# Kernel optimization log

Hardware: AMD Instinct MI355X
Metric: run time of the kernel (lower is better)

Reference implementation:

```python
import jax, jax.numpy as jnp
import numpy as np

N = 8192
LATENT_DIM = 64


def setup_inputs() -> dict:
    key = jax.random.key(0)
    kx, ky = jax.random.split(key)
    x = jax.random.normal(kx, (N, LATENT_DIM), dtype=jnp.float32)
    y = jax.random.normal(ky, (N, LATENT_DIM), dtype=jnp.float32)
    return {"x": x, "y": y}


def _rbf_kernel(a, b):
    # Faithful to torch: exp(-mean((a_i - b_j)^2, axis=dim) / dim)
    #                  = exp(-||a_i - b_j||^2 / dim^2)
    # Computed via the expanded-sq-dist identity to avoid the [N, N, dim]
    # tiled intermediate the torch code materializes.
    dim = a.shape[1]
    sq_a = jnp.sum(a * a, axis=1)  # [Na]
    sq_b = jnp.sum(b * b, axis=1)  # [Nb]
    sq_dist = sq_a[:, None] + sq_b[None, :] - 2.0 * (a @ b.T)  # [Na, Nb]
    return jnp.exp(-sq_dist / (dim * dim))


def reference(x, y):
    # MMD with RBF kernel: mean k(x,x) + mean k(y,y) - 2 mean k(x,y)
    kxx = jnp.mean(_rbf_kernel(x, x))
    kyy = jnp.mean(_rbf_kernel(y, y))
    kxy = jnp.mean(_rbf_kernel(x, y))
    return kxx + kyy - 2.0 * kxy
```

## Files before the change

kernel.cpp:

```cpp
#include <hip/hip_runtime.h>
#include <cmath>

#define NPTS 8192
#define DIM 64
#define BT 128

#define LEAF_F   0
#define LEAF_N   (3 * 8192 * 64)
#define ROWS_F   (LEAF_F + LEAF_N)
#define ROWS_N   (3 * 8192)
#define MEANS_F  (ROWS_F + ROWS_N)
#define NX_F     ((MEANS_F + 3 + 3) & ~3)
#define NY_F     (NX_F + 8192)
#define SPLIT_F  (NY_F + 8192)
#define SPLIT_ELEMS (NPTS * DIM)


typedef short bf16x8 __attribute__((ext_vector_type(8)));
typedef float f32x4  __attribute__((ext_vector_type(4)));

__device__ __forceinline__ unsigned short f32_bf16_rne(float f) {
    unsigned u = __float_as_uint(f);
    return (unsigned short)((u + 0x7FFFu + ((u >> 16) & 1u)) >> 16);
}
__device__ __forceinline__ float bf16_f32(unsigned short h) {
    return __uint_as_float(((unsigned)h) << 16);
}

__device__ __forceinline__ float exp2_hw(float x) {
#if __has_builtin(__builtin_amdgcn_exp2f)
    return __builtin_amdgcn_exp2f(x);
#else
    float r;
    asm("v_exp_f32 %0, %1" : "=v"(r) : "v"(x));
    return r;
#endif
}

#define SWZ_XOR1(x)  __int_as_float(__builtin_amdgcn_ds_swizzle(__float_as_int(x), 0x041F))
#define SWZ_XOR2(x)  __int_as_float(__builtin_amdgcn_ds_swizzle(__float_as_int(x), 0x081F))
#define SWZ_XOR4(x)  __int_as_float(__builtin_amdgcn_ds_swizzle(__float_as_int(x), 0x101F))
#define SWZ_XOR8(x)  __int_as_float(__builtin_amdgcn_ds_swizzle(__float_as_int(x), 0x201F))
#define SWZ_XOR16(x) __int_as_float(__builtin_amdgcn_ds_swizzle(__float_as_int(x), 0x401F))

__global__ void prep_kernel(const float* __restrict__ x, const float* __restrict__ y,
                            unsigned short* __restrict__ Xh, unsigned short* __restrict__ Xl,
                            unsigned short* __restrict__ Yh, unsigned short* __restrict__ Yl,
                            float* __restrict__ nx, float* __restrict__ ny) {
    int gtid = blockIdx.x * 256 + threadIdx.x;
    int r  = gtid >> 4;
    int k4 = gtid & 15;
    int isY = r >= NPTS;
    int rr = isY ? r - NPTS : r;
    const float4* Rg = (const float4*)((isY ? y : x) + (size_t)rr * DIM);
    unsigned short* Hh = isY ? Yh : Xh;
    unsigned short* Hl = isY ? Yl : Xl;
    const int t16 = rr >> 4, mrow = rr & 15;
    float4 v = Rg[k4];
    ushort4 h, l;
    h.x = f32_bf16_rne(v.x); l.x = f32_bf16_rne(v.x - bf16_f32(h.x));
    h.y = f32_bf16_rne(v.y); l.y = f32_bf16_rne(v.y - bf16_f32(h.y));
    h.z = f32_bf16_rne(v.z); l.z = f32_bf16_rne(v.z - bf16_f32(h.z));
    h.w = f32_bf16_rne(v.w); l.w = f32_bf16_rne(v.w - bf16_f32(h.w));
    int off = t16 * 1024 + (k4 >> 3) * 512 + ((k4 >> 1) & 3) * 128 + mrow * 8 + (k4 & 1) * 4;
    *(ushort4*)(Hh + off) = h;
    *(ushort4*)(Hl + off) = l;
    float s = v.x * v.x;
    s = fmaf(v.y, v.y, s); s = fmaf(v.z, v.z, s); s = fmaf(v.w, v.w, s);
    s = s + SWZ_XOR1(s);
    s = s + SWZ_XOR2(s);
    s = s + SWZ_XOR4(s);
    s = s + SWZ_XOR8(s);
    if (k4 == 0) { if (isY) ny[rr] = s; else nx[rr] = s; }
}

__global__ __launch_bounds__(512, 3) void mmd_tile_kernel(
    const unsigned short* __restrict__ Xh, const unsigned short* __restrict__ Xl,
    const unsigned short* __restrict__ Yh, const unsigned short* __restrict__ Yl,
    const float* __restrict__ nx, const float* __restrict__ ny,
    float* __restrict__ leafs)
{
    int id  = blockIdx.x + 65 * (blockIdx.y + 64 * blockIdx.z);
    int nid = (id & 7) * 1040 + (id >> 3);
    int zb  = nid >= 4160;
    int rem = nid - zb * 4160;
    int gj  = rem / 65;
    int gi  = rem - gj * 65;

    int zz, bx, by;
    if (zb == 1) {
        if (gi >= 64) return;
        zz = 2; bx = gi; by = gj;
    } else if (gi > gj) {
        zz = 0; by = gj; bx = gi - 1;
    } else {
        zz = 1; by = gi; bx = gj;
    }

    __shared__ float rowpart[2][BT];
    __shared__ float colpart[4][BT];

    const int t = threadIdx.x;
    const size_t arow = (size_t)by * BT;
    const size_t brow = (size_t)bx * BT;
    const int cb = bx;

    const unsigned short* pAh = (zz == 1) ? Yh : Xh;
    const unsigned short* pAl = (zz == 1) ? Yl : Xl;
    const unsigned short* pBh = (zz == 0) ? Xh : Yh;
    const unsigned short* pBl = (zz == 0) ? Xl : Yl;
    const float* nA = (zz == 1) ? ny : nx;
    const float* nB = (zz == 0) ? nx : ny;

    const int lane = t & 63;
    const int wv   = t >> 6;
    const int mrow = lane & 15;
    const int quad = lane >> 4;
    const int rblk = (wv & 3) << 5;
    const int cblk = (wv >> 2) << 6;

    const int aT = by * 8 + (wv & 3) * 2;
    const int bT = bx * 8 + (wv >> 2) * 4;
    const int lsub = quad * 128 + mrow * 8;

    const bool domirror = (zz < 2) && (bx > by);

    float sa[8];
    #pragma unroll
    for (int rt = 0; rt < 2; ++rt)
        #pragma unroll
        for (int i = 0; i < 4; ++i)
            sa[rt * 4 + i] = nA[arow + rblk + rt * 16 + quad * 4 + i];
    float sb[4];
    #pragma unroll
    for (int ct = 0; ct < 4; ++ct)
        sb[ct] = nB[brow + cblk + ct * 16 + mrow];

    bf16x8 fAh[2][2], fAl[2][2];
    #pragma unroll
    for (int rt = 0; rt < 2; ++rt)
        #pragma unroll
        for (int kc = 0; kc < 2; ++kc) {
            int off = (aT + rt) * 1024 + kc * 512 + lsub;
            fAh[rt][kc] = *(const bf16x8*)(pAh + off);
            fAl[rt][kc] = *(const bf16x8*)(pAl + off);
        }

    bf16x8 fBh0[4], fBh1[4], fBl0[4], fBl1[4];
    #pragma unroll
    for (int ct = 0; ct < 4; ++ct) {
        int boff = (bT + ct) * 1024 + lsub;
        fBh0[ct] = *(const bf16x8*)(pBh + boff);
        fBh1[ct] = *(const bf16x8*)(pBh + boff + 512);
        fBl0[ct] = *(const bf16x8*)(pBl + boff);
        fBl1[ct] = *(const bf16x8*)(pBl + boff + 512);
    }

    const float SCL = (float)(-1.4426950408889634 / 4096.0);
    float rs01[2][4] = {{0.f,0.f,0.f,0.f},{0.f,0.f,0.f,0.f}};
    float rs23[2][4] = {{0.f,0.f,0.f,0.f},{0.f,0.f,0.f,0.f}};
    float cs[4];

    #pragma unroll
    for (int ct = 0; ct < 4; ++ct) {
        bf16x8 bh0 = fBh0[ct];
        bf16x8 bh1 = fBh1[ct];
        bf16x8 bl0 = fBl0[ct];
        bf16x8 bl1 = fBl1[ct];

        f32x4 c0 = (f32x4){0.f, 0.f, 0.f, 0.f};
        f32x4 c1 = (f32x4){0.f, 0.f, 0.f, 0.f};
        __builtin_amdgcn_s_setprio(1);
        c0 = __builtin_amdgcn_mfma_f32_16x16x32_bf16(fAh[0][0], bh0, c0, 0, 0, 0);
        c0 = __builtin_amdgcn_mfma_f32_16x16x32_bf16(fAh[0][0], bl0, c0, 0, 0, 0);
        c0 = __builtin_amdgcn_mfma_f32_16x16x32_bf16(fAl[0][0], bh0, c0, 0, 0, 0);
        c0 = __builtin_amdgcn_mfma_f32_16x16x32_bf16(fAh[0][1], bh1, c0, 0, 0, 0);
        c0 = __builtin_amdgcn_mfma_f32_16x16x32_bf16(fAh[0][1], bl1, c0, 0, 0, 0);
        c0 = __builtin_amdgcn_mfma_f32_16x16x32_bf16(fAl[0][1], bh1, c0, 0, 0, 0);
        c1 = __builtin_amdgcn_mfma_f32_16x16x32_bf16(fAh[1][0], bh0, c1, 0, 0, 0);
        c1 = __builtin_amdgcn_mfma_f32_16x16x32_bf16(fAh[1][0], bl0, c1, 0, 0, 0);
        c1 = __builtin_amdgcn_mfma_f32_16x16x32_bf16(fAl[1][0], bh0, c1, 0, 0, 0);
        c1 = __builtin_amdgcn_mfma_f32_16x16x32_bf16(fAh[1][1], bh1, c1, 0, 0, 0);
        c1 = __builtin_amdgcn_mfma_f32_16x16x32_bf16(fAh[1][1], bl1, c1, 0, 0, 0);
        c1 = __builtin_amdgcn_mfma_f32_16x16x32_bf16(fAl[1][1], bh1, c1, 0, 0, 0);
        __builtin_amdgcn_s_setprio(0);

        float k0[4], k1[4];
        #pragma unroll
        for (int i = 0; i < 4; ++i) {
            float d0  = c0[i];
            float s20 = sa[i] + sb[ct];
            k0[i] = exp2_hw((s20 - 2.0f * d0) * SCL);
            float d1  = c1[i];
            float s21 = sa[4 + i] + sb[ct];
            k1[i] = exp2_hw((s21 - 2.0f * d1) * SCL);
        }
        if (ct < 2) {
            #pragma unroll
            for (int i = 0; i < 4; ++i) { rs01[0][i] += k0[i]; rs01[1][i] += k1[i]; }
        } else {
            #pragma unroll
            for (int i = 0; i < 4; ++i) { rs23[0][i] += k0[i]; rs23[1][i] += k1[i]; }
        }
        if (domirror)
            cs[ct] = ((k0[0] + k0[1]) + (k0[2] + k0[3]))
                   + ((k1[0] + k1[1]) + (k1[2] + k1[3]));
    }

    float rs[2][4];
    #pragma unroll
    for (int rt = 0; rt < 2; ++rt)
        #pragma unroll
        for (int i = 0; i < 4; ++i)
            rs[rt][i] = rs01[rt][i] + rs23[rt][i];

    const int b0 = lane & 1;
    const int b1 = (lane >> 1) & 1;
    const int b2 = (lane >> 2) & 1;
    const int b3 = (lane >> 3) & 1;

    float a4[4];
    #pragma unroll
    for (int i = 0; i < 4; ++i) {
        float snd = b3 ? rs[0][i] : rs[1][i];
        float rcv = SWZ_XOR8(snd);
        a4[i] = (b3 ? rs[1][i] : rs[0][i]) + rcv;
    }
    float a2[2];
    #pragma unroll
    for (int j = 0; j < 2; ++j) {
        float snd = b2 ? a4[j] : a4[2 + j];
        float rcv = SWZ_XOR4(snd);
        a2[j] = (b2 ? a4[2 + j] : a4[j]) + rcv;
    }
    {
        float snd = b1 ? a2[0] : a2[1];
        float rcv = SWZ_XOR2(snd);
        float a1  = (b1 ? a2[1] : a2[0]) + rcv;
        float r64 = a1 + SWZ_XOR1(a1);
        if (b0 == 0)
            rowpart[wv >> 2][rblk + b3 * 16 + quad * 4 + b2 * 2 + b1] = r64;
    }

    if (domirror) {
        const int b4 = (lane >> 4) & 1;
        const int b5 = (lane >> 5) & 1;
        float c2[2];
        #pragma unroll
        for (int j = 0; j < 2; ++j) {
            float snd = b4 ? cs[j] : cs[2 + j];
            float rcv = SWZ_XOR16(snd);
            c2[j] = (b4 ? cs[2 + j] : cs[j]) + rcv;
        }
        float snd = b5 ? c2[0] : c2[1];
        float rcv = __shfl_xor(snd, 32);
        float c1v = (b5 ? c2[1] : c2[0]) + rcv;
        colpart[wv & 3][cblk + (b4 * 2 + b5) * 16 + mrow] = c1v;
    }
    __syncthreads();

    if (t < BT) {
        leafs[((size_t)zz * 64 + cb) * 8192 + arow + t] = rowpart[0][t] + rowpart[1][t];
        if (domirror) {
            leafs[((size_t)zz * 64 + by) * 8192 + brow + t] =
                (colpart[0][t] + colpart[1][t]) + (colpart[2][t] + colpart[3][t]);
        }
    }
}

__global__ void rowsum_kernel(const float* __restrict__ leafs, float* __restrict__ rowsums) {
    const int t = threadIdx.x;
    const int wv = t >> 6;
    const int lane = t & 63;
    const int p = lane >> 4;
    const int rlo = lane & 15;
    const int gr = blockIdx.x * 64 + wv * 16 + rlo;
    const int z = gr >> 13;
    const int r = gr & 8191;
    const float* base = leafs + ((size_t)z * 64 + p * 16) * 8192 + r;
    float v[16];
    #pragma unroll
    for (int i = 0; i < 16; ++i) v[i] = base[(size_t)i * 8192];
    #pragma unroll
    for (int n = 8; n >= 1; n >>= 1)
        #pragma unroll
        for (int i = 0; i < 16; ++i)
            if (i < n) v[i] = v[2*i] + v[2*i+1];
    float s = v[0];
    float u = s + SWZ_XOR16(s);
    float w = u + __shfl_xor(u, 32);
    if (p == 0) rowsums[gr] = w;
}

__global__ void colsum_kernel(const float* __restrict__ rowsums, float* __restrict__ out) {
    __shared__ float L[256];
    __shared__ float m[3];
    const int t = threadIdx.x;
    for (int z = 0; z < 3; ++z) {
        const float4* src = (const float4*)(rowsums + z * 8192);
        float w[32];
        #pragma unroll
        for (int i = 0; i < 8; ++i) {
            float4 q = src[t * 8 + i];
            w[4*i+0] = q.x; w[4*i+1] = q.y; w[4*i+2] = q.z; w[4*i+3] = q.w;
        }
        #pragma unroll
        for (int n = 16; n >= 1; n >>= 1)
            #pragma unroll
            for (int i = 0; i < 32; ++i)
                if (i < n) w[i] = w[2*i] + w[2*i+1];
        L[t] = w[0];
        __syncthreads();
        for (int n = 128; n >= 1; n >>= 1) {
            float u = 0.f;
            if (t < n) u = L[2*t] + L[2*t+1];
            __syncthreads();
            if (t < n) L[t] = u;
            __syncthreads();
        }
        if (t == 0) m[z] = L[0] * (1.0f / 67108864.0f);
        __syncthreads();
    }
    if (t == 0) {
        float t1 = m[0] + m[1];
        out[0] = t1 - 2.0f * m[2];
    }
}

extern "C" void kernel_launch(void* const* d_in, const int* in_sizes, int n_in,
                              void* d_out, int out_size, void* d_ws, size_t ws_size,
                              hipStream_t stream) {
    const float* x = (const float*)d_in[0];
    const float* y = (const float*)d_in[1];
    float* wsf     = (float*)d_ws;
    float* leafs   = wsf + LEAF_F;
    float* rowsums = wsf + ROWS_F;
    float* nx      = wsf + NX_F;
    float* ny      = wsf + NY_F;
    unsigned short* Xh = (unsigned short*)(wsf + SPLIT_F);
    unsigned short* Xl = Xh + SPLIT_ELEMS;
    unsigned short* Yh = Xl + SPLIT_ELEMS;
    unsigned short* Yl = Yh + SPLIT_ELEMS;

    prep_kernel<<<1024, 256, 0, stream>>>(x, y, Xh, Xl, Yh, Yl, nx, ny);
    dim3 grid(65, 64, 2);
    mmd_tile_kernel<<<grid, 512, 0, stream>>>(Xh, Xl, Yh, Yl, nx, ny, leafs);
    rowsum_kernel<<<384, 256, 0, stream>>>(leafs, rowsums);
    colsum_kernel<<<1, 256, 0, stream>>>(rowsums, (float*)d_out);
}
```

Before: 130.5 us.

## Double-buffer B fragments, raise occupancy bound, parallelize colsum over three sums

The tile kernel no longer preloads all four column-tiles of B fragments into registers. It keeps only the current fragment set and prefetches the next one each iteration, and the launch bound is raised from 3 to 6 blocks per SM, both to cut register pressure and allow more waves in flight. The final colsum kernel now reduces the three row-sum arrays concurrently with 768 threads instead of looping over them serially. The tighter register budget risks spills or less latency hiding per wave.

```diff
diff --git a/kernel.cpp b/kernel.cpp
--- a/kernel.cpp
+++ b/kernel.cpp
@@ -74,7 +74,7 @@
     if (k4 == 0) { if (isY) ny[rr] = s; else nx[rr] = s; }
 }
 
-__global__ __launch_bounds__(512, 3) void mmd_tile_kernel(
+__global__ __launch_bounds__(512, 6) void mmd_tile_kernel(
     const unsigned short* __restrict__ Xh, const unsigned short* __restrict__ Xl,
     const unsigned short* __restrict__ Yh, const unsigned short* __restrict__ Yl,
     const float* __restrict__ nx, const float* __restrict__ ny,
@@ -146,43 +146,43 @@
             fAl[rt][kc] = *(const bf16x8*)(pAl + off);
         }
 
-    bf16x8 fBh0[4], fBh1[4], fBl0[4], fBl1[4];
-    #pragma unroll
-    for (int ct = 0; ct < 4; ++ct) {
-        int boff = (bT + ct) * 1024 + lsub;
-        fBh0[ct] = *(const bf16x8*)(pBh + boff);
-        fBh1[ct] = *(const bf16x8*)(pBh + boff + 512);
-        fBl0[ct] = *(const bf16x8*)(pBl + boff);
-        fBl1[ct] = *(const bf16x8*)(pBl + boff + 512);
-    }
-
     const float SCL = (float)(-1.4426950408889634 / 4096.0);
     float rs01[2][4] = {{0.f,0.f,0.f,0.f},{0.f,0.f,0.f,0.f}};
     float rs23[2][4] = {{0.f,0.f,0.f,0.f},{0.f,0.f,0.f,0.f}};
     float cs[4];
 
+    const int boff0 = bT * 1024 + lsub;
+    bf16x8 cbh0 = *(const bf16x8*)(pBh + boff0);
+    bf16x8 cbh1 = *(const bf16x8*)(pBh + boff0 + 512);
+    bf16x8 cbl0 = *(const bf16x8*)(pBl + boff0);
+    bf16x8 cbl1 = *(const bf16x8*)(pBl + boff0 + 512);
+
     #pragma unroll
     for (int ct = 0; ct < 4; ++ct) {
-        bf16x8 bh0 = fBh0[ct];
-        bf16x8 bh1 = fBh1[ct];
-        bf16x8 bl0 = fBl0[ct];
-        bf16x8 bl1 = fBl1[ct];
+        bf16x8 nbh0, nbh1, nbl0, nbl1;
+        if (ct < 3) {
+            int boff = (bT + ct + 1) * 1024 + lsub;
+            nbh0 = *(const bf16x8*)(pBh + boff);
+            nbh1 = *(const bf16x8*)(pBh + boff + 512);
+            nbl0 = *(const bf16x8*)(pBl + boff);
+            nbl1 = *(const bf16x8*)(pBl + boff + 512);
+        }
 
         f32x4 c0 = (f32x4){0.f, 0.f, 0.f, 0.f};
         f32x4 c1 = (f32x4){0.f, 0.f, 0.f, 0.f};
         __builtin_amdgcn_s_setprio(1);
-        c0 = __builtin_amdgcn_mfma_f32_16x16x32_bf16(fAh[0][0], bh0, c0, 0, 0, 0);
-        c0 = __builtin_amdgcn_mfma_f32_16x16x32_bf16(fAh[0][0], bl0, c0, 0, 0, 0);
-        c0 = __builtin_amdgcn_mfma_f32_16x16x32_bf16(fAl[0][0], bh0, c0, 0, 0, 0);
-        c0 = __builtin_amdgcn_mfma_f32_16x16x32_bf16(fAh[0][1], bh1, c0, 0, 0, 0);
-        c0 = __builtin_amdgcn_mfma_f32_16x16x32_bf16(fAh[0][1], bl1, c0, 0, 0, 0);
-        c0 = __builtin_amdgcn_mfma_f32_16x16x32_bf16(fAl[0][1], bh1, c0, 0, 0, 0);
-        c1 = __builtin_amdgcn_mfma_f32_16x16x32_bf16(fAh[1][0], bh0, c1, 0, 0, 0);
-        c1 = __builtin_amdgcn_mfma_f32_16x16x32_bf16(fAh[1][0], bl0, c1, 0, 0, 0);
-        c1 = __builtin_amdgcn_mfma_f32_16x16x32_bf16(fAl[1][0], bh0, c1, 0, 0, 0);
-        c1 = __builtin_amdgcn_mfma_f32_16x16x32_bf16(fAh[1][1], bh1, c1, 0, 0, 0);
-        c1 = __builtin_amdgcn_mfma_f32_16x16x32_bf16(fAh[1][1], bl1, c1, 0, 0, 0);
-        c1 = __builtin_amdgcn_mfma_f32_16x16x32_bf16(fAl[1][1], bh1, c1, 0, 0, 0);
+        c0 = __builtin_amdgcn_mfma_f32_16x16x32_bf16(fAh[0][0], cbh0, c0, 0, 0, 0);
+        c0 = __builtin_amdgcn_mfma_f32_16x16x32_bf16(fAh[0][0], cbl0, c0, 0, 0, 0);
+        c0 = __builtin_amdgcn_mfma_f32_16x16x32_bf16(fAl[0][0], cbh0, c0, 0, 0, 0);
+        c0 = __builtin_amdgcn_mfma_f32_16x16x32_bf16(fAh[0][1], cbh1, c0, 0, 0, 0);
+        c0 = __builtin_amdgcn_mfma_f32_16x16x32_bf16(fAh[0][1], cbl1, c0, 0, 0, 0);
+        c0 = __builtin_amdgcn_mfma_f32_16x16x32_bf16(fAl[0][1], cbh1, c0, 0, 0, 0);
+        c1 = __builtin_amdgcn_mfma_f32_16x16x32_bf16(fAh[1][0], cbh0, c1, 0, 0, 0);
+        c1 = __builtin_amdgcn_mfma_f32_16x16x32_bf16(fAh[1][0], cbl0, c1, 0, 0, 0);
+        c1 = __builtin_amdgcn_mfma_f32_16x16x32_bf16(fAl[1][0], cbh0, c1, 0, 0, 0);
+        c1 = __builtin_amdgcn_mfma_f32_16x16x32_bf16(fAh[1][1], cbh1, c1, 0, 0, 0);
+        c1 = __builtin_amdgcn_mfma_f32_16x16x32_bf16(fAh[1][1], cbl1, c1, 0, 0, 0);
+        c1 = __builtin_amdgcn_mfma_f32_16x16x32_bf16(fAl[1][1], cbh1, c1, 0, 0, 0);
         __builtin_amdgcn_s_setprio(0);
 
         float k0[4], k1[4];
@@ -205,6 +205,10 @@
         if (domirror)
             cs[ct] = ((k0[0] + k0[1]) + (k0[2] + k0[3]))
                    + ((k1[0] + k1[1]) + (k1[2] + k1[3]));
+
+        if (ct < 3) {
+            cbh0 = nbh0; cbh1 = nbh1; cbl0 = nbl0; cbl1 = nbl1;
+        }
     }
 
     float rs[2][4];
@@ -293,15 +297,17 @@
 }
 
 __global__ void colsum_kernel(const float* __restrict__ rowsums, float* __restrict__ out) {
-    __shared__ float L[256];
+    __shared__ float L[3][256];
     __shared__ float m[3];
-    const int t = threadIdx.x;
-    for (int z = 0; z < 3; ++z) {
+    const int t  = threadIdx.x;
+    const int z  = t >> 8;
+    const int tz = t & 255;
+    {
         const float4* src = (const float4*)(rowsums + z * 8192);
         float w[32];
         #pragma unroll
         for (int i = 0; i < 8; ++i) {
-            float4 q = src[t * 8 + i];
+            float4 q = src[tz * 8 + i];
             w[4*i+0] = q.x; w[4*i+1] = q.y; w[4*i+2] = q.z; w[4*i+3] = q.w;
         }
         #pragma unroll
@@ -309,18 +315,18 @@
             #pragma unroll
             for (int i = 0; i < 32; ++i)
                 if (i < n) w[i] = w[2*i] + w[2*i+1];
-        L[t] = w[0];
+        L[z][tz] = w[0];
+    }
+    __syncthreads();
+    for (int n = 128; n >= 1; n >>= 1) {
+        float u = 0.f;
+        if (tz < n) u = L[z][2*tz] + L[z][2*tz+1];
         __syncthreads();
-        for (int n = 128; n >= 1; n >>= 1) {
-            float u = 0.f;
-            if (t < n) u = L[2*t] + L[2*t+1];
-            __syncthreads();
-            if (t < n) L[t] = u;
-            __syncthreads();
-        }
-        if (t == 0) m[z] = L[0] * (1.0f / 67108864.0f);
+        if (tz < n) L[z][tz] = u;
         __syncthreads();
     }
+    if (tz == 0) m[z] = L[z][0] * (1.0f / 67108864.0f);
+    __syncthreads();
     if (t == 0) {
         float t1 = m[0] + m[1];
         out[0] = t1 - 2.0f * m[2];
@@ -346,5 +352,5 @@
     dim3 grid(65, 64, 2);
     mmd_tile_kernel<<<grid, 512, 0, stream>>>(Xh, Xl, Yh, Yl, nx, ny, leafs);
     rowsum_kernel<<<384, 256, 0, stream>>>(leafs, rowsums);
-    colsum_kernel<<<1, 256, 0, stream>>>(rowsums, (float*)d_out);
-}
+    colsum_kernel<<<1, 768, 0, stream>>>(rowsums, (float*)d_out);
+}
```

Measured after the change: 468.7 us. 259% more time.
